# Kernel tuning notes

Measured on AMD Instinct MI355X. Metric: run time of the kernel, lower is better.

Reference implementation:

```python
import jax, jax.numpy as jnp
import numpy as np

N_HEADS = 16

def setup_inputs() -> dict:
    key = jax.random.key(0)
    k1, k2 = jax.random.split(key)
    qkv = jax.random.normal(k1, (2, 3072, 2048), dtype=jnp.float32)
    encoder_kv = jax.random.normal(k2, (2, 2048, 512), dtype=jnp.float32)
    return {"qkv": qkv, "encoder_kv": encoder_kv}

def reference(qkv, encoder_kv):
    bs, width, length = qkv.shape
    ch = width // (3 * N_HEADS)  # 64
    # [bs*H, 3*ch, T] -> q, k, v each [bs*H, ch, T]
    qkv_r = qkv.reshape(bs * N_HEADS, ch * 3, length)
    q, k, v = qkv_r[:, :ch], qkv_r[:, ch:2 * ch], qkv_r[:, 2 * ch:]
    # encoder kv: [bs*H, 2*ch, S] -> ek, ev; prepend to k/v along token axis
    ekv = encoder_kv.reshape(bs * N_HEADS, ch * 2, -1)
    ek, ev = ekv[:, :ch], ekv[:, ch:]
    k = jnp.concatenate([ek, k], axis=-1)  # [bs*H, ch, S+T]
    v = jnp.concatenate([ev, v], axis=-1)
    scale = 1.0 / (ch ** 0.25)  # split pre-scaling as in original
    weight = jnp.einsum('bct,bcs->bts', q * scale, k * scale)  # [bs*H, T, S+T]
    weight = jax.nn.softmax(weight.astype(jnp.float32), axis=-1).astype(weight.dtype)
    a = jnp.einsum('bts,bcs->bct', weight, v)  # [bs*H, ch, T]
    return a.reshape(bs, -1, length)
```

## Files before the change

### kernel.cpp

```cpp
#include <hip/hip_runtime.h>


#define QT_BYTES (32u * 2048u * 128u)
#define KV_TILE  16384
#define N_ST     40

typedef _Float16 h4 __attribute__((ext_vector_type(4)));
typedef _Float16 h8 __attribute__((ext_vector_type(8)));
typedef __fp16   g2 __attribute__((ext_vector_type(2)));
typedef float    f4 __attribute__((ext_vector_type(4)));

typedef __attribute__((address_space(1))) const unsigned int GAS;
typedef __attribute__((address_space(3))) unsigned int LAS;

static __device__ __forceinline__ void dma16(const void* g, void* l) {
    __builtin_amdgcn_global_load_lds((GAS*)g, (LAS*)l, 16, 0, 0);
}

static __device__ __forceinline__ unsigned short f2h(float f) {
    union { _Float16 h; unsigned short u; } v;
    v.h = (_Float16)f;
    return v.u;
}

__global__ __launch_bounds__(256) void prep_kernel(
        const float* __restrict__ qkv,
        const float* __restrict__ ekv,
        char* __restrict__ ws) {
    __shared__ __align__(16) unsigned short sT[64 * 80];
    const int tid = threadIdx.x;

    const int x = blockIdx.x & 7;
    const int i = blockIdx.x >> 3;

    if (i < 288) {
        const float* src; int stride; char* dst; float scale;
        if (i < 128) {
            int bh = x * 4 + (i >> 5), tt = i & 31;
            int b = bh >> 4, h = bh & 15;
            src = qkv + (size_t)b * 6291456 + (size_t)(h * 192) * 2048 + tt * 64;
            stride = 2048;
            dst = ws + (size_t)bh * 262144 + (size_t)tt * 8192;
            scale = 0.18033688f;
        } else {
            int j = i - 128; int bh = x * 4 + j / 40, st = j % 40;
            int b = bh >> 4, h = bh & 15;
            if (st < 8) { src = ekv + (size_t)b * 1048576 + (size_t)(h * 128) * 512 + st * 64; stride = 512; }
            else        { src = qkv + (size_t)b * 6291456 + (size_t)(h * 192 + 64) * 2048 + (size_t)(st - 8) * 64; stride = 2048; }
            dst = ws + QT_BYTES + ((size_t)bh * 40 + st) * KV_TILE;
            scale = 1.0f;
        }
        const int c = tid >> 2, t4 = (tid & 3) * 16;
        #pragma unroll
        for (int k = 0; k < 4; ++k) {
            int t = t4 + k * 4;
            float4 v = *(const float4*)(src + (size_t)c * stride + t);
            sT[(t + 0) * 80 + c] = f2h(v.x * scale);
            sT[(t + 1) * 80 + c] = f2h(v.y * scale);
            sT[(t + 2) * 80 + c] = f2h(v.z * scale);
            sT[(t + 3) * 80 + c] = f2h(v.w * scale);
        }
        __syncthreads();
        #pragma unroll
        for (int ii = 0; ii < 2; ++ii) {
            int idx = tid * 2 + ii;
            int r = idx >> 3, pc = idx & 7;
            int lc = pc ^ (r & 7);
            *(uint4*)(dst + r * 128 + pc * 16) = *(const uint4*)(sT + r * 80 + lc * 8);
        }
    } else {
        int j = i - 288; int bh = x * 4 + j / 40, st = j % 40;
        int b = bh >> 4, h = bh & 15;
        const float* src; int stride;
        if (st < 8) { src = ekv + (size_t)b * 1048576 + (size_t)(h * 128 + 64) * 512 + st * 64; stride = 512; }
        else        { src = qkv + (size_t)b * 6291456 + (size_t)(h * 192 + 128) * 2048 + (size_t)(st - 8) * 64; stride = 2048; }
        char* dst = ws + QT_BYTES + ((size_t)bh * 40 + st) * KV_TILE + 8192;
        const int c = tid >> 2, s16 = (tid & 3) * 16;
        #pragma unroll
        for (int g = 0; g < 2; ++g) {
            float4 a  = *(const float4*)(src + (size_t)c * stride + s16 + g * 8);
            float4 bb = *(const float4*)(src + (size_t)c * stride + s16 + g * 8 + 4);
            unsigned int u0 = (unsigned int)f2h(a.x)  | ((unsigned int)f2h(a.y)  << 16);
            unsigned int u1 = (unsigned int)f2h(a.z)  | ((unsigned int)f2h(a.w)  << 16);
            unsigned int u2 = (unsigned int)f2h(bb.x) | ((unsigned int)f2h(bb.y) << 16);
            unsigned int u3 = (unsigned int)f2h(bb.z) | ((unsigned int)f2h(bb.w) << 16);
            int pc = ((s16 >> 3) + g) ^ (c & 7);
            uint4 pk = {u0, u1, u2, u3};
            *(uint4*)(dst + c * 128 + pc * 16) = pk;
        }
    }
}

__global__ __launch_bounds__(512, 4) void attn_fwd(
        const char* __restrict__ ws,
        float* __restrict__ out) {
    __shared__ __align__(16) char smem[81920];
    char* sQ = smem;

    const int tid = threadIdx.x;
    const int w = tid >> 6, lane = tid & 63;
    const int pair = w >> 1;
    const int par  = w & 1;
    const int sub  = w >> 1;
    const int quad = lane >> 4, nn = lane & 15;

    const int lid = blockIdx.x;
    const int bh = (lid & 7) * 4 + (lid >> 7);
    const int t0 = ((lid >> 3) & 15) * 128;
    const int b = bh >> 4, h = bh & 15;

    const char* qsrc  = ws + (size_t)bh * 262144 + (size_t)t0 * 128;
    const char* kvsrc = ws + QT_BYTES + (size_t)bh * 40 * KV_TILE;

    #pragma unroll
    for (int i = 0; i < 2; ++i) {
        int off = (w * 2 + i) * 1024;
        dma16(qsrc + off + lane * 16, sQ + off);
    }
    #pragma unroll
    for (int i = 0; i < 4; ++i) {
        int off = (sub * 4 + i) * 1024;
        dma16(kvsrc + (size_t)par * KV_TILE + off + lane * 16,
              smem + 16384 + par * 16384 + off);
    }
    __syncthreads();

    h8 qb[2][2];
    #pragma unroll
    for (int nt = 0; nt < 2; ++nt) {
        int r = pair * 32 + nt * 16 + nn;
        #pragma unroll
        for (int kh = 0; kh < 2; ++kh)
            qb[nt][kh] = *(const h8*)(sQ + r * 128 + (((kh * 4 + quad) ^ (nn & 7)) * 16));
    }

    f4 o[2][4];
    float lsum[2];
    #pragma unroll
    for (int nt = 0; nt < 2; ++nt) {
        lsum[nt] = 0.f;
        #pragma unroll
        for (int cm = 0; cm < 4; ++cm) {
            o[nt][cm][0] = 0.f; o[nt][cm][1] = 0.f; o[nt][cm][2] = 0.f; o[nt][cm][3] = 0.f;
        }
    }
    const int sw = nn & 7;

    for (int it = 0; it < N_ST / 2; ++it) {
        char* cur = smem + 16384 + ((it & 1) * 2 + par) * 16384;
        if (it < N_ST / 2 - 1) {
            char* nxt = smem + 16384 + ((((it + 1) & 1) * 2) + par) * 16384;
            const char* g = kvsrc + (size_t)(2 * (it + 1) + par) * KV_TILE;
            #pragma unroll
            for (int i = 0; i < 4; ++i) {
                int off = (sub * 4 + i) * 1024;
                dma16(g + off + lane * 16, nxt + off);
            }
        }
        const char* sK = cur;
        const char* sV = cur + 8192;

        #pragma unroll
        for (int ct = 0; ct < 4; ++ct) {
            h8 ka0 = *(const h8*)(sK + (ct * 16 + nn) * 128 + ((quad ^ sw) * 16));
            h8 ka1 = *(const h8*)(sK + (ct * 16 + nn) * 128 + (((4 + quad) ^ sw) * 16));
            h4 va[4];
            {
                int lc = 2 * ct + (quad >> 1);
                int vo = ((lc ^ sw) * 16) + (quad & 1) * 8;
                #pragma unroll
                for (int cm = 0; cm < 4; ++cm)
                    va[cm] = *(const h4*)(sV + (cm * 16 + nn) * 128 + vo);
            }
            #pragma unroll
            for (int nt = 0; nt < 2; ++nt) {
                f4 z = {0.f, 0.f, 0.f, 0.f};
                z = __builtin_amdgcn_mfma_f32_16x16x32_f16(ka0, qb[nt][0], z, 0, 0, 0);
                z = __builtin_amdgcn_mfma_f32_16x16x32_f16(ka1, qb[nt][1], z, 0, 0, 0);
                float e0 = __builtin_amdgcn_exp2f(z[0]);
                float e1 = __builtin_amdgcn_exp2f(z[1]);
                float e2 = __builtin_amdgcn_exp2f(z[2]);
                float e3 = __builtin_amdgcn_exp2f(z[3]);
                lsum[nt] += (e0 + e1) + (e2 + e3);
                union { g2 g[2]; h4 h; } pu;
                pu.g[0] = __builtin_amdgcn_cvt_pkrtz(e0, e1);
                pu.g[1] = __builtin_amdgcn_cvt_pkrtz(e2, e3);
                h4 pb = pu.h;
                #pragma unroll
                for (int cm = 0; cm < 4; ++cm)
                    o[nt][cm] = __builtin_amdgcn_mfma_f32_16x16x16f16(va[cm], pb, o[nt][cm], 0, 0, 0);
            }
        }
        __syncthreads();
    }

    #pragma unroll
    for (int nt = 0; nt < 2; ++nt) {
        lsum[nt] += __shfl_xor(lsum[nt], 16);
        lsum[nt] += __shfl_xor(lsum[nt], 32);
    }

    char* scr = smem + pair * 10240;
    if (par == 1) {
        #pragma unroll
        for (int nt = 0; nt < 2; ++nt) {
            #pragma unroll
            for (int cm = 0; cm < 4; ++cm)
                *(f4*)(scr + (nt * 4 + cm) * 1024 + lane * 16) = o[nt][cm];
            *(float*)(scr + 8192 + nt * 256 + lane * 4) = lsum[nt];
        }
    }
    __syncthreads();
    if (par == 0) {
        float* outp = out + (size_t)b * 2097152 + (size_t)(h * 64) * 2048 + t0;
        #pragma unroll
        for (int nt = 0; nt < 2; ++nt) {
            float pl = *(const float*)(scr + 8192 + nt * 256 + lane * 4);
            float rl = 1.0f / (lsum[nt] + pl);
            int t = pair * 32 + nt * 16 + nn;
            #pragma unroll
            for (int cm = 0; cm < 4; ++cm) {
                f4 po = *(const f4*)(scr + (nt * 4 + cm) * 1024 + lane * 16);
                #pragma unroll
                for (int r2 = 0; r2 < 4; ++r2) {
                    int c = cm * 16 + quad * 4 + r2;
                    outp[(size_t)c * 2048 + t] = (o[nt][cm][r2] + po[r2]) * rl;
                }
            }
        }
    }
}

extern "C" void kernel_launch(void* const* d_in, const int* in_sizes, int n_in,
                              void* d_out, int out_size, void* d_ws, size_t ws_size,
                              hipStream_t stream) {
    const float* qkv = (const float*)d_in[0];
    const float* ekv = (const float*)d_in[1];
    float* out = (float*)d_out;
    char* ws = (char*)d_ws;

    prep_kernel<<<3584, 256, 0, stream>>>(qkv, ekv, ws);
    attn_fwd<<<512, 512, 0, stream>>>(ws, out);
}
```

Before: 149.3 us.

## Halve query tile per block, split channel tiles across wave pairs

Each block now handles 64 query rows instead of 128, and the grid doubles to 1024 blocks. Shared memory drops to 32KB because Q is loaded straight from global into registers. The KV tiles are double-buffered one at a time, and the two waves of a pair split the key columns within each tile rather than alternating whole tiles. The aim is better occupancy and load balance across CUs. The cost is twice the total KV traffic, since each block streams the full KV for fewer queries.

Measured after the change: 162.4 us. +8.8%, slower.

```diff
diff --git a/kernel.cpp b/kernel.cpp
--- a/kernel.cpp
+++ b/kernel.cpp
@@ -91,141 +91,112 @@
     }
 }
 
-__global__ __launch_bounds__(512, 4) void attn_fwd(
+__global__ __launch_bounds__(512, 8) void attn_fwd(
         const char* __restrict__ ws,
         float* __restrict__ out) {
-    __shared__ __align__(16) char smem[81920];
-    char* sQ = smem;
+    __shared__ __align__(16) char smem[32768];
 
     const int tid = threadIdx.x;
     const int w = tid >> 6, lane = tid & 63;
-    const int pair = w >> 1;
-    const int par  = w & 1;
-    const int sub  = w >> 1;
+    const int tq = w >> 1;
+    const int sh = w & 1;
     const int quad = lane >> 4, nn = lane & 15;
 
     const int lid = blockIdx.x;
-    const int bh = (lid & 7) * 4 + (lid >> 7);
-    const int t0 = ((lid >> 3) & 15) * 128;
+    const int bh = (lid & 7) * 4 + (lid >> 8);
+    const int t0 = ((lid >> 3) & 31) * 64;
     const int b = bh >> 4, h = bh & 15;
 
     const char* qsrc  = ws + (size_t)bh * 262144 + (size_t)t0 * 128;
     const char* kvsrc = ws + QT_BYTES + (size_t)bh * 40 * KV_TILE;
 
+    const int off = w * 2048;
+    dma16(kvsrc + off + lane * 16,        smem + off);
+    dma16(kvsrc + off + 1024 + lane * 16, smem + off + 1024);
+
+    h8 qb[2];
+    {
+        int r = tq * 16 + nn;
+        #pragma unroll
+        for (int kh = 0; kh < 2; ++kh)
+            qb[kh] = *(const h8*)(qsrc + r * 128 + (((kh * 4 + quad) ^ (nn & 7)) * 16));
+    }
+    __syncthreads();
+
+    f4 o[4];
+    float lsum = 0.f;
     #pragma unroll
-    for (int i = 0; i < 2; ++i) {
-        int off = (w * 2 + i) * 1024;
-        dma16(qsrc + off + lane * 16, sQ + off);
-    }
-    #pragma unroll
-    for (int i = 0; i < 4; ++i) {
-        int off = (sub * 4 + i) * 1024;
-        dma16(kvsrc + (size_t)par * KV_TILE + off + lane * 16,
-              smem + 16384 + par * 16384 + off);
-    }
-    __syncthreads();
-
-    h8 qb[2][2];
-    #pragma unroll
-    for (int nt = 0; nt < 2; ++nt) {
-        int r = pair * 32 + nt * 16 + nn;
-        #pragma unroll
-        for (int kh = 0; kh < 2; ++kh)
-            qb[nt][kh] = *(const h8*)(sQ + r * 128 + (((kh * 4 + quad) ^ (nn & 7)) * 16));
-    }
-
-    f4 o[2][4];
-    float lsum[2];
-    #pragma unroll
-    for (int nt = 0; nt < 2; ++nt) {
-        lsum[nt] = 0.f;
-        #pragma unroll
-        for (int cm = 0; cm < 4; ++cm) {
-            o[nt][cm][0] = 0.f; o[nt][cm][1] = 0.f; o[nt][cm][2] = 0.f; o[nt][cm][3] = 0.f;
-        }
+    for (int cm = 0; cm < 4; ++cm) {
+        o[cm][0] = 0.f; o[cm][1] = 0.f; o[cm][2] = 0.f; o[cm][3] = 0.f;
     }
     const int sw = nn & 7;
 
-    for (int it = 0; it < N_ST / 2; ++it) {
-        char* cur = smem + 16384 + ((it & 1) * 2 + par) * 16384;
-        if (it < N_ST / 2 - 1) {
-            char* nxt = smem + 16384 + ((((it + 1) & 1) * 2) + par) * 16384;
-            const char* g = kvsrc + (size_t)(2 * (it + 1) + par) * KV_TILE;
-            #pragma unroll
-            for (int i = 0; i < 4; ++i) {
-                int off = (sub * 4 + i) * 1024;
-                dma16(g + off + lane * 16, nxt + off);
-            }
+    for (int j = 0; j < N_ST; ++j) {
+        const char* cur = smem + (j & 1) * 16384;
+        if (j < N_ST - 1) {
+            char* nxt = smem + ((j + 1) & 1) * 16384;
+            const char* g = kvsrc + (size_t)(j + 1) * KV_TILE;
+            dma16(g + off + lane * 16,        nxt + off);
+            dma16(g + off + 1024 + lane * 16, nxt + off + 1024);
         }
         const char* sK = cur;
         const char* sV = cur + 8192;
 
         #pragma unroll
-        for (int ct = 0; ct < 4; ++ct) {
-            h8 ka0 = *(const h8*)(sK + (ct * 16 + nn) * 128 + ((quad ^ sw) * 16));
-            h8 ka1 = *(const h8*)(sK + (ct * 16 + nn) * 128 + (((4 + quad) ^ sw) * 16));
+        for (int cs = 0; cs < 2; ++cs) {
+            const int ct = sh * 2 + cs;
+            const int krow = (ct * 16 + nn) * 128;
+            h8 ka0 = *(const h8*)(sK + krow + ((quad ^ sw) * 16));
+            h8 ka1 = *(const h8*)(sK + krow + (((4 + quad) ^ sw) * 16));
             h4 va[4];
             {
-                int lc = 2 * ct + (quad >> 1);
-                int vo = ((lc ^ sw) * 16) + (quad & 1) * 8;
+                int vo = (((2 * ct + (quad >> 1)) ^ sw) * 16) + (quad & 1) * 8;
                 #pragma unroll
                 for (int cm = 0; cm < 4; ++cm)
                     va[cm] = *(const h4*)(sV + (cm * 16 + nn) * 128 + vo);
             }
-            #pragma unroll
-            for (int nt = 0; nt < 2; ++nt) {
-                f4 z = {0.f, 0.f, 0.f, 0.f};
-                z = __builtin_amdgcn_mfma_f32_16x16x32_f16(ka0, qb[nt][0], z, 0, 0, 0);
-                z = __builtin_amdgcn_mfma_f32_16x16x32_f16(ka1, qb[nt][1], z, 0, 0, 0);
-                float e0 = __builtin_amdgcn_exp2f(z[0]);
-                float e1 = __builtin_amdgcn_exp2f(z[1]);
-                float e2 = __builtin_amdgcn_exp2f(z[2]);
-                float e3 = __builtin_amdgcn_exp2f(z[3]);
-                lsum[nt] += (e0 + e1) + (e2 + e3);
-                union { g2 g[2]; h4 h; } pu;
-                pu.g[0] = __builtin_amdgcn_cvt_pkrtz(e0, e1);
-                pu.g[1] = __builtin_amdgcn_cvt_pkrtz(e2, e3);
-                h4 pb = pu.h;
-                #pragma unroll
-                for (int cm = 0; cm < 4; ++cm)
-                    o[nt][cm] = __builtin_amdgcn_mfma_f32_16x16x16f16(va[cm], pb, o[nt][cm], 0, 0, 0);
-            }
-        }
-        __syncthreads();
-    }
-
-    #pragma unroll
-    for (int nt = 0; nt < 2; ++nt) {
-        lsum[nt] += __shfl_xor(lsum[nt], 16);
-        lsum[nt] += __shfl_xor(lsum[nt], 32);
-    }
-
-    char* scr = smem + pair * 10240;
-    if (par == 1) {
-        #pragma unroll
-        for (int nt = 0; nt < 2; ++nt) {
+            f4 z = {0.f, 0.f, 0.f, 0.f};
+            z = __builtin_amdgcn_mfma_f32_16x16x32_f16(ka0, qb[0], z, 0, 0, 0);
+            z = __builtin_amdgcn_mfma_f32_16x16x32_f16(ka1, qb[1], z, 0, 0, 0);
+            float e0 = __builtin_amdgcn_exp2f(z[0]);
+            float e1 = __builtin_amdgcn_exp2f(z[1]);
+            float e2 = __builtin_amdgcn_exp2f(z[2]);
+            float e3 = __builtin_amdgcn_exp2f(z[3]);
+            lsum += (e0 + e1) + (e2 + e3);
+            union { g2 g[2]; h4 h; } pu;
+            pu.g[0] = __builtin_amdgcn_cvt_pkrtz(e0, e1);
+            pu.g[1] = __builtin_amdgcn_cvt_pkrtz(e2, e3);
+            h4 pb = pu.h;
             #pragma unroll
             for (int cm = 0; cm < 4; ++cm)
-                *(f4*)(scr + (nt * 4 + cm) * 1024 + lane * 16) = o[nt][cm];
-            *(float*)(scr + 8192 + nt * 256 + lane * 4) = lsum[nt];
-        }
+                o[cm] = __builtin_amdgcn_mfma_f32_16x16x16f16(va[cm], pb, o[cm], 0, 0, 0);
+        }
+        __syncthreads();
+    }
+
+    lsum += __shfl_xor(lsum, 16);
+    lsum += __shfl_xor(lsum, 32);
+
+    char* scr = smem + tq * 4352;
+    if (sh == 1) {
+        #pragma unroll
+        for (int cm = 0; cm < 4; ++cm)
+            *(f4*)(scr + cm * 1024 + lane * 16) = o[cm];
+        *(float*)(scr + 4096 + lane * 4) = lsum;
     }
     __syncthreads();
-    if (par == 0) {
+    if (sh == 0) {
         float* outp = out + (size_t)b * 2097152 + (size_t)(h * 64) * 2048 + t0;
-        #pragma unroll
-        for (int nt = 0; nt < 2; ++nt) {
-            float pl = *(const float*)(scr + 8192 + nt * 256 + lane * 4);
-            float rl = 1.0f / (lsum[nt] + pl);
-            int t = pair * 32 + nt * 16 + nn;
+        float pl = *(const float*)(scr + 4096 + lane * 4);
+        float rl = 1.0f / (lsum + pl);
+        int t = tq * 16 + nn;
+        #pragma unroll
+        for (int cm = 0; cm < 4; ++cm) {
+            f4 po = *(const f4*)(scr + cm * 1024 + lane * 16);
             #pragma unroll
-            for (int cm = 0; cm < 4; ++cm) {
-                f4 po = *(const f4*)(scr + (nt * 4 + cm) * 1024 + lane * 16);
-                #pragma unroll
-                for (int r2 = 0; r2 < 4; ++r2) {
-                    int c = cm * 16 + quad * 4 + r2;
-                    outp[(size_t)c * 2048 + t] = (o[nt][cm][r2] + po[r2]) * rl;
-                }
+            for (int r2 = 0; r2 < 4; ++r2) {
+                int c = cm * 16 + quad * 4 + r2;
+                outp[(size_t)c * 2048 + t] = (o[cm][r2] + po[r2]) * rl;
             }
         }
     }
@@ -240,5 +211,5 @@
     char* ws = (char*)d_ws;
 
     prep_kernel<<<3584, 256, 0, stream>>>(qkv, ekv, ws);
-    attn_fwd<<<512, 512, 0, stream>>>(ws, out);
-}
+    attn_fwd<<<1024, 512, 0, stream>>>(ws, out);
+}
```
